# Kernel tuning notes

Measured on AMD Instinct MI355X. Metric: run time of the kernel, lower is better.

The kernel has to match this reference:

```python
import jax, jax.numpy as jnp
import numpy as np

N, E, F_IN = 50000, 800000, 128
H, C, CLS, G = 8, 32, 16, 64
NEG_SLOPE = 0.2


def setup_inputs() -> dict:
    key = jax.random.key(0)
    ks = jax.random.split(key, 11)
    s = 0.05
    return {
        "x": jax.random.normal(ks[0], (N, F_IN), jnp.float32),
        "edge_index": jax.random.randint(ks[1], (2, E), 0, N, jnp.int32),
        "batch": jnp.sort(jax.random.randint(ks[2], (N,), 0, G, jnp.int32)),
        "W1": jax.random.normal(ks[3], (F_IN, H * C), jnp.float32) * s,
        "a1_src": jax.random.normal(ks[4], (H, C), jnp.float32) * s,
        "a1_dst": jax.random.normal(ks[5], (H, C), jnp.float32) * s,
        "b1": jax.random.normal(ks[6], (H * C,), jnp.float32) * s,
        "W2": jax.random.normal(ks[7], (H * C, CLS), jnp.float32) * s,
        "a2_src": jax.random.normal(ks[8], (1, CLS), jnp.float32) * s,
        "a2_dst": jax.random.normal(ks[9], (1, CLS), jnp.float32) * s,
        "b2": jax.random.normal(ks[10], (CLS,), jnp.float32) * s,
    }


def _gat_conv(x, src, dst, W, a_s, a_d, b, concat):
    n = x.shape[0]
    Hh, Cc = a_s.shape
    xp = (x @ W).reshape(n, Hh, Cc)                      # [N,H,C]
    al_s = jnp.einsum("nhc,hc->nh", xp, a_s)             # [N,H]
    al_d = jnp.einsum("nhc,hc->nh", xp, a_d)
    e = jax.nn.leaky_relu(al_s[src] + al_d[dst], NEG_SLOPE)  # [E,H]
    m = jax.ops.segment_max(e, dst, num_segments=n)      # segment softmax over dst
    ex = jnp.exp(e - m[dst])
    denom = jax.ops.segment_sum(ex, dst, num_segments=n)
    alpha = ex / denom[dst]                              # [E,H]
    out = jax.ops.segment_sum(xp[src] * alpha[:, :, None], dst, num_segments=n)
    out = out.reshape(n, Hh * Cc) if concat else out.mean(axis=1)
    return out + b


def reference(x, edge_index, batch, W1, a1_src, a1_dst, b1, W2, a2_src, a2_dst, b2):
    n = x.shape[0]
    loops = jnp.arange(n, dtype=edge_index.dtype)        # PyG add_self_loops=True
    ei = jnp.concatenate([edge_index, jnp.stack([loops, loops])], axis=1)
    src, dst = ei[0], ei[1]
    h = jax.nn.elu(_gat_conv(x, src, dst, W1, a1_src, a1_dst, b1, True))
    h = _gat_conv(h, src, dst, W2, a2_src, a2_dst, b2, False)
    counts = jax.ops.segment_sum(jnp.ones((n,), h.dtype), batch, num_segments=G)
    pooled = jax.ops.segment_sum(h, batch, num_segments=G) / jnp.maximum(counts, 1.0)[:, None]
    return jax.nn.log_softmax(pooled, axis=1)
```

## Files before the change

kernel.cpp:

```cpp
#include <hip/hip_runtime.h>
#include <math.h>

#define N_NODES 50000
#define N_EDGES 800000
#define FDIM 128
#define NH 8
#define NC 32
#define D1 256
#define NCLS 16
#define NGRP 64
#define NEG 0.2f
#define E_TOT (N_EDGES + N_NODES)
#define NB_N 196
#define G1_BLOCKS 782
#define E_CHUNK 4096
#define NCHUNK 196
#define NBIN 196

typedef __attribute__((ext_vector_type(4))) unsigned short u16x4;
typedef __attribute__((ext_vector_type(8))) unsigned short u16x8;
typedef __attribute__((ext_vector_type(8))) short short8;
typedef __attribute__((ext_vector_type(4))) float f32x4;

static __device__ __forceinline__ float bf2f(unsigned short u) {
    return __uint_as_float(((unsigned int)u) << 16);
}
static __device__ __forceinline__ unsigned short f2bf(float f) {
    unsigned int b = __float_as_uint(f);
    return (unsigned short)((b + 0x7FFFu + ((b >> 16) & 1u)) >> 16);
}

__global__ __launch_bounds__(256) void k_init(
    const float* __restrict__ W1, unsigned short* __restrict__ w1p,
    float* __restrict__ poolS, float* __restrict__ poolC,
    const int* __restrict__ ei, int* __restrict__ binmat) {
    __shared__ int h[NBIN];
    int c = blockIdx.x;
    for (int b = threadIdx.x; b < NBIN; b += 256) h[b] = 0;
    __syncthreads();
    int e0 = c * E_CHUNK;
    int e1 = e0 + E_CHUNK; if (e1 > N_EDGES) e1 = N_EDGES;
    for (int e = e0 + threadIdx.x; e < e1; e += 256)
        atomicAdd(&h[ei[N_EDGES + e] >> 8], 1);
    int i = blockIdx.x * 256 + threadIdx.x;
    if (i < NGRP * NCLS) poolS[i] = 0.f;
    if (i < NGRP) poolC[i] = 0.f;
    if (i < FDIM * D1) {
        int ks = i >> 13;
        int r = i & 8191;
        int nt2 = r >> 9;
        int r2 = r & 511;
        int lane = r2 >> 3, e = r2 & 7;
        int k = ks * 32 + (lane >> 4) * 8 + e;
        int col = nt2 * 16 + (lane & 15);
        w1p[i] = f2bf(W1[k * D1 + col]);
    }
    __syncthreads();
    for (int b = threadIdx.x; b < NBIN; b += 256) binmat[b * NCHUNK + c] = h[b];
}

__global__ __launch_bounds__(256) void k_binprescan(int* __restrict__ binmat,
                                                    int* __restrict__ binTot) {
    __shared__ int sh[256];
    int b = blockIdx.x, t = threadIdx.x;
    int v = (t < NCHUNK) ? binmat[b * NCHUNK + t] : 0;
    sh[t] = v;
    __syncthreads();
    for (int d = 1; d < 256; d <<= 1) {
        int tv = (t >= d) ? sh[t - d] : 0;
        __syncthreads();
        sh[t] += tv;
        __syncthreads();
    }
    if (t < NCHUNK) binmat[b * NCHUNK + t] = sh[t] - v;
    if (t == 255) binTot[b] = sh[255];
}

__global__ __launch_bounds__(256) void k_gemm1m(
    const float* __restrict__ x, const unsigned short* __restrict__ w1p,
    const float* __restrict__ a1s, const float* __restrict__ a1d,
    unsigned short* __restrict__ xp1b, float* __restrict__ al1s,
    float* __restrict__ al1d) {
    const int l = threadIdx.x & 63;
    const int wid = threadIdx.x >> 6;
    const int wr = wid >> 1, wc = wid & 1;
    const int l15 = l & 15, l4 = l >> 4;
    const int base = blockIdx.x * 64;
    const int r0 = base + wr * 32;

    f32x4 acc[2][8] = {};
#pragma unroll
    for (int ks = 0; ks < 4; ++ks) {
        const int kk = ks * 32 + l4 * 8;
        short8 af[2];
#pragma unroll
        for (int rt = 0; rt < 2; ++rt) {
            int row = r0 + rt * 16 + l15;
            float4 v0 = make_float4(0.f, 0.f, 0.f, 0.f), v1 = v0;
            if (row < N_NODES) {
                const float* xr = x + (size_t)row * FDIM + kk;
                v0 = *(const float4*)xr;
                v1 = *(const float4*)(xr + 4);
            }
            short8 a;
            a[0] = (short)f2bf(v0.x); a[1] = (short)f2bf(v0.y);
            a[2] = (short)f2bf(v0.z); a[3] = (short)f2bf(v0.w);
            a[4] = (short)f2bf(v1.x); a[5] = (short)f2bf(v1.y);
            a[6] = (short)f2bf(v1.z); a[7] = (short)f2bf(v1.w);
            af[rt] = a;
        }
#pragma unroll
        for (int nt = 0; nt < 8; ++nt) {
            int nt2 = wc * 8 + nt;
            short8 bf_ = *(const short8*)&w1p[(size_t)((ks * 16 + nt2) * 64 + l) * 8];
            acc[0][nt] = __builtin_amdgcn_mfma_f32_16x16x32_bf16(af[0], bf_, acc[0][nt], 0, 0, 0);
            acc[1][nt] = __builtin_amdgcn_mfma_f32_16x16x32_bf16(af[1], bf_, acc[1][nt], 0, 0, 0);
        }
    }
#pragma unroll
    for (int rt = 0; rt < 2; ++rt) {
        int rbase = r0 + rt * 16 + l4 * 4;
#pragma unroll
        for (int nt = 0; nt < 8; ++nt) {
            int col = wc * 128 + nt * 16 + l15;
            f32x4 c = acc[rt][nt];
#pragma unroll
            for (int r = 0; r < 4; ++r) {
                int row = rbase + r;
                if (row < N_NODES) xp1b[(size_t)row * D1 + col] = f2bf(c[r]);
            }
        }
    }
#pragma unroll
    for (int hl = 0; hl < 4; ++hl) {
        int hg = wc * 4 + hl;
        float as0 = a1s[hg * NC + l15], as1 = a1s[hg * NC + 16 + l15];
        float ad0 = a1d[hg * NC + l15], ad1 = a1d[hg * NC + 16 + l15];
#pragma unroll
        for (int rt = 0; rt < 2; ++rt) {
            f32x4 c0 = acc[rt][2 * hl], c1 = acc[rt][2 * hl + 1];
#pragma unroll
            for (int r = 0; r < 4; ++r) {
                float ss = c0[r] * as0 + c1[r] * as1;
                float dd = c0[r] * ad0 + c1[r] * ad1;
#pragma unroll
                for (int msk = 1; msk < 16; msk <<= 1) {
                    ss += __shfl_xor(ss, msk);
                    dd += __shfl_xor(dd, msk);
                }
                int row = r0 + rt * 16 + l4 * 4 + r;
                if (l15 == 0 && row < N_NODES) {
                    al1s[row * NH + hg] = ss;
                    al1d[row * NH + hg] = dd;
                }
            }
        }
    }
}

__global__ __launch_bounds__(256) void k_binscatter(const int* __restrict__ ei,
                                                    const int* __restrict__ offs,
                                                    const int* __restrict__ binTot,
                                                    int* __restrict__ binned) {
    __shared__ int cur[NBIN];
    __shared__ int sb[256];
    int c = blockIdx.x;
    int t = threadIdx.x;
    int v = (t < NBIN) ? binTot[t] : 0;
    sb[t] = v;
    __syncthreads();
    for (int d = 1; d < 256; d <<= 1) {
        int tv = (t >= d) ? sb[t - d] : 0;
        __syncthreads();
        sb[t] += tv;
        __syncthreads();
    }
    if (t < NBIN) cur[t] = (sb[t] - v) + offs[t * NCHUNK + c];
    __syncthreads();
    int e0 = c * E_CHUNK;
    int e1 = e0 + E_CHUNK; if (e1 > N_EDGES) e1 = N_EDGES;
    for (int e = e0 + t; e < e1; e += 256) {
        int s = ei[e], d = ei[N_EDGES + e];
        int pos = atomicAdd(&cur[d >> 8], 1);
        binned[pos] = s | ((d & 255) << 16);
    }
}

__global__ __launch_bounds__(256) void k_bincsr(const int* __restrict__ binTot,
                                                const int* __restrict__ binned,
                                                int* __restrict__ rowptr,
                                                int* __restrict__ cnt,
                                                int* __restrict__ esrc) {
    __shared__ int sh[256];
    __shared__ int lcnt[256];
    __shared__ int lcur[256];
    int b = blockIdx.x;
    int t = threadIdx.x;
    int v = (t < NBIN) ? binTot[t] : 0;
    sh[t] = v;
    __syncthreads();
    for (int d = 1; d < 256; d <<= 1) {
        int tv = (t >= d) ? sh[t - d] : 0;
        __syncthreads();
        sh[t] += tv;
        __syncthreads();
    }
    int estart = (b == 0) ? 0 : sh[b - 1];
    int eend = sh[b];
    __syncthreads();
    int nbase = b * 256;
    int nin = N_NODES - nbase; if (nin > 256) nin = 256;
    lcnt[t] = 0;
    __syncthreads();
    for (int e = estart + t; e < eend; e += 256)
        atomicAdd(&lcnt[(binned[e] >> 16) & 255], 1);
    __syncthreads();
    int myc = lcnt[t] + (t < nin ? 1 : 0);
    sh[t] = myc;
    __syncthreads();
    for (int d = 1; d < 256; d <<= 1) {
        int tv = (t >= d) ? sh[t - d] : 0;
        __syncthreads();
        sh[t] += tv;
        __syncthreads();
    }
    int excl = sh[t] - myc;
    int outbase = estart + nbase;
    int rp = outbase + excl;
    if (t < nin) {
        rowptr[nbase + t] = rp;
        cnt[nbase + t] = myc;
        esrc[rp] = nbase + t;
    }
    lcur[t] = rp + (t < nin ? 1 : 0);
    __syncthreads();
    for (int e = estart + t; e < eend; e += 256) {
        int vv = binned[e];
        int pos = atomicAdd(&lcur[(vv >> 16) & 255], 1);
        esrc[pos] = vv & 0xFFFF;
    }
}

__global__ __launch_bounds__(256) void k_att1f(
    const unsigned short* __restrict__ xp1b, const float* __restrict__ al1s,
    const float* __restrict__ al1d, const float* __restrict__ b1,
    const float* __restrict__ W2, const float* __restrict__ a2s,
    const float* __restrict__ a2d, const int* __restrict__ rowptr,
    const int* __restrict__ cnt, const int* __restrict__ esrc,
    float* __restrict__ xp2, float* __restrict__ al2s, float* __restrict__ al2d) {
    __shared__ int s_src[4][64];
    __shared__ float s_alpha[4][64 * 8];
    int wv = threadIdx.x >> 6;
    int lane = threadIdx.x & 63;
    int n = blockIdx.x * 4 + wv;
    int start = rowptr[n];
    int deg = cnt[n];
    int dcap = deg < 64 ? deg : 64;
    int dpad = (dcap + 7) & ~7;
    for (int j = lane; j < dpad; j += 64)
        s_src[wv][j] = (j < dcap) ? esrc[start + j] : n;
    int npad = (dpad - dcap) * 8;
    if (lane < npad) s_alpha[wv][dcap * 8 + lane] = 0.f;
    int h = lane & 7, eg = lane >> 3;
    float ald = al1d[n * NH + h];
    float m = -1e30f;
    for (int j = eg; j < dcap; j += 8) {
        int s = s_src[wv][j];
        float v = al1s[s * NH + h] + ald;
        v = fmaxf(v, NEG * v);
        s_alpha[wv][j * 8 + h] = v;
        m = fmaxf(m, v);
    }
    if (deg > 64) {
        for (int j = 64 + eg; j < deg; j += 8) {
            int s = esrc[start + j];
            float v = al1s[s * NH + h] + ald;
            m = fmaxf(m, fmaxf(v, NEG * v));
        }
    }
    for (int msk = 8; msk < 64; msk <<= 1) m = fmaxf(m, __shfl_xor(m, msk));
    float den = 0.f;
    for (int j = eg; j < dcap; j += 8) {
        float e = __expf(s_alpha[wv][j * 8 + h] - m);
        s_alpha[wv][j * 8 + h] = e;
        den += e;
    }
    if (deg > 64) {
        for (int j = 64 + eg; j < deg; j += 8) {
            int s = esrc[start + j];
            float v = al1s[s * NH + h] + ald;
            v = fmaxf(v, NEG * v);
            den += __expf(v - m);
        }
    }
    for (int msk = 8; msk < 64; msk <<= 1) den += __shfl_xor(den, msk);
    int eh = lane >> 5;
    int l5 = lane & 31;
    int h2 = l5 >> 2;
    float rd2 = 1.f / __shfl(den, h2);
    float m2 = __shfl(m, h2);
    const int cbb = l5 << 4;
    float acc[8] = {0.f, 0.f, 0.f, 0.f, 0.f, 0.f, 0.f, 0.f};
    for (int j0 = 0; j0 < dpad; j0 += 8) {
        int off[4];
        float aw[4];
#pragma unroll
        for (int k = 0; k < 4; ++k) {
            int e = j0 + eh + 2 * k;
            int s = s_src[wv][e];
            aw[k] = s_alpha[wv][e * 8 + h2];
            off[k] = (s << 9) + cbb;
        }
#pragma unroll
        for (int k = 0; k < 4; ++k) {
            u16x8 xv = *(const u16x8*)((const char*)xp1b + off[k]);
#pragma unroll
            for (int c = 0; c < 8; ++c) acc[c] = fmaf(aw[k], bf2f(xv[c]), acc[c]);
        }
    }
    if (deg > 64) {
        float ald2 = al1d[n * NH + h2];
        for (int j = 64 + eh; j < deg; j += 2) {
            int s = esrc[start + j];
            float v = al1s[s * NH + h2] + ald2;
            v = fmaxf(v, NEG * v);
            float al = __expf(v - m2);
            u16x8 xv = *(const u16x8*)((const char*)xp1b + (s << 9) + cbb);
#pragma unroll
            for (int c = 0; c < 8; ++c) acc[c] = fmaf(al, bf2f(xv[c]), acc[c]);
        }
    }
#pragma unroll
    for (int c = 0; c < 8; ++c) acc[c] += __shfl_xor(acc[c], 32);
    float* h_l = &s_alpha[wv][0];
    if (eh == 0) {
        int cb = l5 << 3;
        float4 b0 = *(const float4*)(b1 + cb);
        float4 b4 = *(const float4*)(b1 + cb + 4);
        float r0_ = fmaf(acc[0], rd2, b0.x);
        float r1_ = fmaf(acc[1], rd2, b0.y);
        float r2_ = fmaf(acc[2], rd2, b0.z);
        float r3_ = fmaf(acc[3], rd2, b0.w);
        float r4_ = fmaf(acc[4], rd2, b4.x);
        float r5_ = fmaf(acc[5], rd2, b4.y);
        float r6_ = fmaf(acc[6], rd2, b4.z);
        float r7_ = fmaf(acc[7], rd2, b4.w);
        r0_ = r0_ > 0.f ? r0_ : expm1f(r0_);
        r1_ = r1_ > 0.f ? r1_ : expm1f(r1_);
        r2_ = r2_ > 0.f ? r2_ : expm1f(r2_);
        r3_ = r3_ > 0.f ? r3_ : expm1f(r3_);
        r4_ = r4_ > 0.f ? r4_ : expm1f(r4_);
        r5_ = r5_ > 0.f ? r5_ : expm1f(r5_);
        r6_ = r6_ > 0.f ? r6_ : expm1f(r6_);
        r7_ = r7_ > 0.f ? r7_ : expm1f(r7_);
        *(float4*)&h_l[cb]     = make_float4(r0_, r1_, r2_, r3_);
        *(float4*)&h_l[cb + 4] = make_float4(r4_, r5_, r6_, r7_);
    }
    {
        int o = lane & 15, q = lane >> 4;
        const float* hq = h_l + q * 4;
        const float* wq = W2 + q * 64 + o;
        float po0 = 0.f, po1 = 0.f, po2 = 0.f, po3 = 0.f;
#pragma unroll
        for (int cc = 0; cc < 16; ++cc) {
            float4 hv = *(const float4*)(hq + cc * 16);
            const float* w = wq + cc * 256;
            po0 = fmaf(hv.x, w[0],  po0);
            po1 = fmaf(hv.y, w[16], po1);
            po2 = fmaf(hv.z, w[32], po2);
            po3 = fmaf(hv.w, w[48], po3);
        }
        float po = (po0 + po1) + (po2 + po3);
        po += __shfl_xor(po, 16);
        po += __shfl_xor(po, 32);
        float ts = po * a2s[o];
        float td = po * a2d[o];
#pragma unroll
        for (int msk = 1; msk < 16; msk <<= 1) {
            ts += __shfl_xor(ts, msk);
            td += __shfl_xor(td, msk);
        }
        if (lane < 16) xp2[(size_t)n * NCLS + lane] = po;
        if (lane == 0) { al2s[n] = ts; al2d[n] = td; }
    }
}

__global__ __launch_bounds__(256) void k_att2(
    const float* __restrict__ xp2, const float* __restrict__ al2s,
    const float* __restrict__ al2d, const float* __restrict__ b2,
    const int* __restrict__ rowptr, const int* __restrict__ cnt,
    const int* __restrict__ esrc, float* __restrict__ out2) {
    __shared__ int s_src[4][64];
    __shared__ float s_a[4][64];
    int wave = threadIdx.x >> 6;
    int lane = threadIdx.x & 63;
    int n = blockIdx.x * 4 + wave;
    int start = rowptr[n];
    int deg = cnt[n];
    int dcap = deg < 64 ? deg : 64;
    int dpad = (dcap + 7) & ~7;
    for (int j = lane; j < dpad; j += 64)
        s_src[wave][j] = (j < dcap) ? esrc[start + j] : n;
    if (lane < dpad - dcap) s_a[wave][dcap + lane] = 0.f;
    float ald = al2d[n];
    float m = -1e30f;
    for (int j = lane; j < dcap; j += 64) {
        int s = s_src[wave][j];
        float v = al2s[s] + ald;
        v = fmaxf(v, NEG * v);
        s_a[wave][j] = v;
        m = fmaxf(m, v);
    }
    if (deg > 64) {
        for (int j = 64 + lane; j < deg; j += 64) {
            float v = al2s[esrc[start + j]] + ald;
            m = fmaxf(m, fmaxf(v, NEG * v));
        }
    }
    for (int msk = 1; msk < 64; msk <<= 1) m = fmaxf(m, __shfl_xor(m, msk));
    float den = 0.f;
    for (int j = lane; j < dcap; j += 64) {
        float e = __expf(s_a[wave][j] - m);
        s_a[wave][j] = e;
        den += e;
    }
    if (deg > 64) {
        for (int j = 64 + lane; j < deg; j += 64) {
            float v = al2s[esrc[start + j]] + ald;
            v = fmaxf(v, NEG * v);
            den += __expf(v - m);
        }
    }
    for (int msk = 1; msk < 64; msk <<= 1) den += __shfl_xor(den, msk);
    float rden = 1.f / den;
    int c = lane & 15;
    int eg = lane >> 4;
    float acc = 0.f;
    for (int j0 = 0; j0 < dpad; j0 += 8) {
#pragma unroll
        for (int k = 0; k < 2; ++k) {
            int e = j0 + eg + 4 * k;
            float aw = s_a[wave][e];
            int s = s_src[wave][e];
            acc = fmaf(aw, xp2[(size_t)s * NCLS + c], acc);
        }
    }
    if (deg > 64) {
        for (int j = 64 + eg; j < deg; j += 4) {
            int s = esrc[start + j];
            float v = al2s[s] + ald;
            v = fmaxf(v, NEG * v);
            acc += __expf(v - m) * xp2[(size_t)s * NCLS + c];
        }
    }
    acc += __shfl_xor(acc, 16);
    acc += __shfl_xor(acc, 32);
    if (lane < 16) out2[(size_t)n * NCLS + lane] = acc * rden + b2[lane];
}

__global__ __launch_bounds__(256) void k_pool(
    const float* __restrict__ out2, const int* __restrict__ batch,
    float* __restrict__ poolS, float* __restrict__ poolC) {
    __shared__ float sacc[NGRP * NCLS];
    __shared__ float scnt[NGRP];
    for (int i = threadIdx.x; i < NGRP * NCLS; i += 256) sacc[i] = 0.f;
    if (threadIdx.x < NGRP) scnt[threadIdx.x] = 0.f;
    __syncthreads();
    int n = blockIdx.x * 256 + threadIdx.x;
    if (n < N_NODES) {
        int g = batch[n];
        atomicAdd(&scnt[g], 1.f);
#pragma unroll
        for (int q = 0; q < 4; ++q) {
            float4 v = *(const float4*)(out2 + (size_t)n * NCLS + q * 4);
            atomicAdd(&sacc[g * NCLS + q * 4 + 0], v.x);
            atomicAdd(&sacc[g * NCLS + q * 4 + 1], v.y);
            atomicAdd(&sacc[g * NCLS + q * 4 + 2], v.z);
            atomicAdd(&sacc[g * NCLS + q * 4 + 3], v.w);
        }
    }
    __syncthreads();
    for (int i = threadIdx.x; i < NGRP * NCLS; i += 256)
        if (sacc[i] != 0.f) atomicAdd(&poolS[i], sacc[i]);
    if (threadIdx.x < NGRP && scnt[threadIdx.x] != 0.f)
        atomicAdd(&poolC[threadIdx.x], scnt[threadIdx.x]);
}

__global__ void k_final(const float* __restrict__ poolS,
                        const float* __restrict__ poolC, float* __restrict__ out) {
    int g = threadIdx.x;
    if (g >= NGRP) return;
    float inv = 1.f / fmaxf(poolC[g], 1.f);
    float v[NCLS];
    float m = -1e30f;
#pragma unroll
    for (int c = 0; c < NCLS; ++c) {
        v[c] = poolS[g * NCLS + c] * inv;
        m = fmaxf(m, v[c]);
    }
    float s = 0.f;
#pragma unroll
    for (int c = 0; c < NCLS; ++c) s += expf(v[c] - m);
    float lse = m + logf(s);
#pragma unroll
    for (int c = 0; c < NCLS; ++c) out[g * NCLS + c] = v[c] - lse;
}

extern "C" void kernel_launch(void* const* d_in, const int* in_sizes, int n_in,
                              void* d_out, int out_size, void* d_ws, size_t ws_size,
                              hipStream_t stream) {
    const float* x    = (const float*)d_in[0];
    const int*   ei   = (const int*)d_in[1];
    const int*   batch = (const int*)d_in[2];
    const float* W1   = (const float*)d_in[3];
    const float* a1s  = (const float*)d_in[4];
    const float* a1d  = (const float*)d_in[5];
    const float* b1   = (const float*)d_in[6];
    const float* W2   = (const float*)d_in[7];
    const float* a2s  = (const float*)d_in[8];
    const float* a2d  = (const float*)d_in[9];
    const float* b2   = (const float*)d_in[10];
    float* out = (float*)d_out;

    float* f = (float*)d_ws;
    float* al1s_ = f;  f += (size_t)N_NODES * NH;
    float* al1d_ = f;  f += (size_t)N_NODES * NH;
    float* xp2   = f;  f += (size_t)N_NODES * NCLS;
    float* al2s_ = f;  f += N_NODES;
    float* al2d_ = f;  f += N_NODES;
    float* out2  = f;  f += (size_t)N_NODES * NCLS;
    float* poolS = f;  f += NGRP * NCLS;
    float* poolC = f;  f += NGRP;
    unsigned short* xp1b = (unsigned short*)f;
    unsigned short* w1p  = xp1b + (size_t)N_NODES * D1;
    int* binmat  = (int*)(w1p + FDIM * D1);
    int* binTot  = binmat + NBIN * NCHUNK;
    int* binned  = binTot + NBIN;
    int* rowptr  = binned + N_EDGES;
    int* cnt     = rowptr + N_NODES;
    int* esrc    = cnt + N_NODES;

    k_init<<<NB_N, 256, 0, stream>>>(W1, w1p, poolS, poolC, ei, binmat);
    k_binprescan<<<NBIN, 256, 0, stream>>>(binmat, binTot);
    k_gemm1m<<<G1_BLOCKS, 256, 0, stream>>>(x, w1p, a1s, a1d, xp1b, al1s_, al1d_);
    k_binscatter<<<NCHUNK, 256, 0, stream>>>(ei, binmat, binTot, binned);
    k_bincsr<<<NBIN, 256, 0, stream>>>(binTot, binned, rowptr, cnt, esrc);
    k_att1f<<<N_NODES / 4, 256, 0, stream>>>(xp1b, al1s_, al1d_, b1, W2, a2s, a2d,
                                             rowptr, cnt, esrc, xp2, al2s_, al2d_);
    k_att2<<<N_NODES / 4, 256, 0, stream>>>(xp2, al2s_, al2d_, b2, rowptr, cnt, esrc, out2);
    k_pool<<<NB_N, 256, 0, stream>>>(out2, batch, poolS, poolC);
    k_final<<<1, 64, 0, stream>>>(poolS, poolC, out);
}
```

Measured before the change: 188.4 us.

## Merge edge binning scatter into GEMM launch and store layer-2 features as bf16

```diff
diff --git a/kernel.cpp b/kernel.cpp
--- a/kernel.cpp
+++ b/kernel.cpp
@@ -80,7 +80,34 @@
     const float* __restrict__ x, const unsigned short* __restrict__ w1p,
     const float* __restrict__ a1s, const float* __restrict__ a1d,
     unsigned short* __restrict__ xp1b, float* __restrict__ al1s,
-    float* __restrict__ al1d) {
+    float* __restrict__ al1d, const int* __restrict__ ei,
+    const int* __restrict__ offs, const int* __restrict__ binTot,
+    int* __restrict__ binned) {
+    __shared__ int cur[NBIN];
+    __shared__ int sb[256];
+    if (blockIdx.x >= G1_BLOCKS) {
+        int c = blockIdx.x - G1_BLOCKS;
+        int t = threadIdx.x;
+        int v = (t < NBIN) ? binTot[t] : 0;
+        sb[t] = v;
+        __syncthreads();
+        for (int d = 1; d < 256; d <<= 1) {
+            int tv = (t >= d) ? sb[t - d] : 0;
+            __syncthreads();
+            sb[t] += tv;
+            __syncthreads();
+        }
+        if (t < NBIN) cur[t] = (sb[t] - v) + offs[t * NCHUNK + c];
+        __syncthreads();
+        int e0 = c * E_CHUNK;
+        int e1 = e0 + E_CHUNK; if (e1 > N_EDGES) e1 = N_EDGES;
+        for (int e = e0 + t; e < e1; e += 256) {
+            int s = ei[e], d = ei[N_EDGES + e];
+            int pos = atomicAdd(&cur[d >> 8], 1);
+            binned[pos] = s | ((d & 255) << 16);
+        }
+        return;
+    }
     const int l = threadIdx.x & 63;
     const int wid = threadIdx.x >> 6;
     const int wr = wid >> 1, wc = wid & 1;
@@ -158,34 +185,6 @@
     }
 }
 
-__global__ __launch_bounds__(256) void k_binscatter(const int* __restrict__ ei,
-                                                    const int* __restrict__ offs,
-                                                    const int* __restrict__ binTot,
-                                                    int* __restrict__ binned) {
-    __shared__ int cur[NBIN];
-    __shared__ int sb[256];
-    int c = blockIdx.x;
-    int t = threadIdx.x;
-    int v = (t < NBIN) ? binTot[t] : 0;
-    sb[t] = v;
-    __syncthreads();
-    for (int d = 1; d < 256; d <<= 1) {
-        int tv = (t >= d) ? sb[t - d] : 0;
-        __syncthreads();
-        sb[t] += tv;
-        __syncthreads();
-    }
-    if (t < NBIN) cur[t] = (sb[t] - v) + offs[t * NCHUNK + c];
-    __syncthreads();
-    int e0 = c * E_CHUNK;
-    int e1 = e0 + E_CHUNK; if (e1 > N_EDGES) e1 = N_EDGES;
-    for (int e = e0 + t; e < e1; e += 256) {
-        int s = ei[e], d = ei[N_EDGES + e];
-        int pos = atomicAdd(&cur[d >> 8], 1);
-        binned[pos] = s | ((d & 255) << 16);
-    }
-}
-
 __global__ __launch_bounds__(256) void k_bincsr(const int* __restrict__ binTot,
                                                 const int* __restrict__ binned,
                                                 int* __restrict__ rowptr,
@@ -247,7 +246,8 @@
     const float* __restrict__ W2, const float* __restrict__ a2s,
     const float* __restrict__ a2d, const int* __restrict__ rowptr,
     const int* __restrict__ cnt, const int* __restrict__ esrc,
-    float* __restrict__ xp2, float* __restrict__ al2s, float* __restrict__ al2d) {
+    unsigned short* __restrict__ xp2b, float* __restrict__ al2s,
+    float* __restrict__ al2d) {
     __shared__ int s_src[4][64];
     __shared__ float s_alpha[4][64 * 8];
     int wv = threadIdx.x >> 6;
@@ -380,13 +380,13 @@
             ts += __shfl_xor(ts, msk);
             td += __shfl_xor(td, msk);
         }
-        if (lane < 16) xp2[(size_t)n * NCLS + lane] = po;
+        if (lane < 16) xp2b[(size_t)n * NCLS + lane] = f2bf(po);
         if (lane == 0) { al2s[n] = ts; al2d[n] = td; }
     }
 }
 
 __global__ __launch_bounds__(256) void k_att2(
-    const float* __restrict__ xp2, const float* __restrict__ al2s,
+    const unsigned short* __restrict__ xp2b, const float* __restrict__ al2s,
     const float* __restrict__ al2d, const float* __restrict__ b2,
     const int* __restrict__ rowptr, const int* __restrict__ cnt,
     const int* __restrict__ esrc, float* __restrict__ out2) {
@@ -442,7 +442,7 @@
             int e = j0 + eg + 4 * k;
             float aw = s_a[wave][e];
             int s = s_src[wave][e];
-            acc = fmaf(aw, xp2[(size_t)s * NCLS + c], acc);
+            acc = fmaf(aw, bf2f(xp2b[(size_t)s * NCLS + c]), acc);
         }
     }
     if (deg > 64) {
@@ -450,7 +450,7 @@
             int s = esrc[start + j];
             float v = al2s[s] + ald;
             v = fmaxf(v, NEG * v);
-            acc += __expf(v - m) * xp2[(size_t)s * NCLS + c];
+            acc += __expf(v - m) * bf2f(xp2b[(size_t)s * NCLS + c]);
         }
     }
     acc += __shfl_xor(acc, 16);
@@ -525,14 +525,14 @@
     float* f = (float*)d_ws;
     float* al1s_ = f;  f += (size_t)N_NODES * NH;
     float* al1d_ = f;  f += (size_t)N_NODES * NH;
-    float* xp2   = f;  f += (size_t)N_NODES * NCLS;
     float* al2s_ = f;  f += N_NODES;
     float* al2d_ = f;  f += N_NODES;
     float* out2  = f;  f += (size_t)N_NODES * NCLS;
     float* poolS = f;  f += NGRP * NCLS;
     float* poolC = f;  f += NGRP;
     unsigned short* xp1b = (unsigned short*)f;
-    unsigned short* w1p  = xp1b + (size_t)N_NODES * D1;
+    unsigned short* xp2b = xp1b + (size_t)N_NODES * D1;
+    unsigned short* w1p  = xp2b + (size_t)N_NODES * NCLS;
     int* binmat  = (int*)(w1p + FDIM * D1);
     int* binTot  = binmat + NBIN * NCHUNK;
     int* binned  = binTot + NBIN;
@@ -542,12 +542,13 @@
 
     k_init<<<NB_N, 256, 0, stream>>>(W1, w1p, poolS, poolC, ei, binmat);
     k_binprescan<<<NBIN, 256, 0, stream>>>(binmat, binTot);
-    k_gemm1m<<<G1_BLOCKS, 256, 0, stream>>>(x, w1p, a1s, a1d, xp1b, al1s_, al1d_);
-    k_binscatter<<<NCHUNK, 256, 0, stream>>>(ei, binmat, binTot, binned);
+    k_gemm1m<<<G1_BLOCKS + NCHUNK, 256, 0, stream>>>(x, w1p, a1s, a1d, xp1b,
+                                                     al1s_, al1d_, ei, binmat,
+                                                     binTot, binned);
     k_bincsr<<<NBIN, 256, 0, stream>>>(binTot, binned, rowptr, cnt, esrc);
     k_att1f<<<N_NODES / 4, 256, 0, stream>>>(xp1b, al1s_, al1d_, b1, W2, a2s, a2d,
-                                             rowptr, cnt, esrc, xp2, al2s_, al2d_);
-    k_att2<<<N_NODES / 4, 256, 0, stream>>>(xp2, al2s_, al2d_, b2, rowptr, cnt, esrc, out2);
+                                             rowptr, cnt, esrc, xp2b, al2s_, al2d_);
+    k_att2<<<N_NODES / 4, 256, 0, stream>>>(xp2b, al2s_, al2d_, b2, rowptr, cnt, esrc, out2);
     k_pool<<<NB_N, 256, 0, stream>>>(out2, batch, poolS, poolC);
     k_final<<<1, 64, 0, stream>>>(poolS, poolC, out);
 }
```

Measured after the change: 170.5 us, median of 2. 1.1x faster.
